# Optimization experiments

Hardware: AMD Instinct MI355X
Metric: run time of the kernel (lower is better)

## Reference

```python
import jax, jax.numpy as jnp
import numpy as np
import math

VOCAB = 128000
D_MODEL = 1024
CUTOFFS = [20000, 60000, VOCAB]  # cluster boundaries (last = vocab_size)
B, S = 8, 4096


def setup_inputs() -> dict:
    key = jax.random.key(0)
    ks = jax.random.split(key, 6)
    input_ids = jax.random.randint(ks[0], (B, S), 0, VOCAB)
    # cluster 0: ids [0, 20000), dim 1024, padding_idx=0 -> zero row
    emb0 = jax.random.normal(ks[1], (20000, 1024), jnp.float32)
    emb0 = emb0.at[0].set(0.0)
    # cluster 1: ids [20000, 60000), dim 256 (= 1024 // 4**1)
    emb1 = jax.random.normal(ks[2], (40000, 256), jnp.float32)
    # cluster 2: ids [60000, 128000), dim 64 (= 1024 // 4**2)
    emb2 = jax.random.normal(ks[3], (68000, 64), jnp.float32)
    # nn.Linear(emb_dim, d_model, bias=False): weight shape [d_model, emb_dim]
    proj1 = jax.random.normal(ks[4], (1024, 256), jnp.float32) * 0.02
    proj2 = jax.random.normal(ks[5], (1024, 64), jnp.float32) * 0.02
    return {"input_ids": input_ids, "emb0": emb0, "emb1": emb1, "emb2": emb2,
            "proj1": proj1, "proj2": proj2}


def reference(input_ids, emb0, emb1, emb2, proj1, proj2):
    d_model = emb0.shape[1]
    starts = [0, CUTOFFS[0], CUTOFFS[1]]
    ends = CUTOFFS
    tables = [emb0, emb1, emb2]
    projs = [None, proj1, proj2]
    out = jnp.zeros(input_ids.shape + (d_model,), jnp.float32)
    for start, end, tab, proj in zip(starts, ends, tables, projs):
        mask = (input_ids >= start) & (input_ids < end)          # [B,S]
        local = jnp.clip(input_ids - start, 0, tab.shape[0] - 1)  # in-range gather ids
        e = tab[local]                                            # [B,S,emb_dim]
        if proj is not None:
            e = jnp.einsum('bse,de->bsd', e, proj)                # project to d_model
        else:
            # padding_idx=0: row is zero; mask keeps grad out of row 0 too
            e = e * (input_ids != 0)[..., None].astype(e.dtype)
        out = out + jnp.where(mask[..., None], e, 0.0)            # masked scatter
    return out * math.sqrt(d_model)
```

## Files before the change

### kernel.cpp

```cpp
#include <hip/hip_runtime.h>
#include <hip/hip_bf16.h>


typedef __attribute__((ext_vector_type(4))) float        float4v;
typedef __attribute__((ext_vector_type(8))) short        short8;
typedef __attribute__((ext_vector_type(2))) unsigned int uint2v;

#define D_MODEL 1024

__device__ __forceinline__ short f2bf(float x) {
    unsigned u = __builtin_bit_cast(unsigned, x);
    unsigned r = u + 0x7fffu + ((u >> 16) & 1u);
    return (short)(r >> 16);
}

__device__ __forceinline__ uint2v pack4(float4v v) {
    uint2v r;
    r[0] = (unsigned)(unsigned short)f2bf(v[0]) | ((unsigned)(unsigned short)f2bf(v[1]) << 16);
    r[1] = (unsigned)(unsigned short)f2bf(v[2]) | ((unsigned)(unsigned short)f2bf(v[3]) << 16);
    return r;
}

__global__ __launch_bounds__(1024)
void prep_k(const int* __restrict__ ids, int n, int pb,
            int* __restrict__ cnt,
            int* __restrict__ l0, int* __restrict__ l1, int* __restrict__ l2,
            const float* __restrict__ proj1, const float* __restrict__ proj2,
            uint2v* __restrict__ p1bf, uint2v* __restrict__ p2bf)
{
    const int b = blockIdx.x;
    if (b >= pb) {
        int bb = b - pb;
        if (bb < 64) {
            int t = bb * 1024 + threadIdx.x;
            p1bf[t] = pack4(((const float4v*)proj1)[t]);
        } else {
            int t = (bb - 64) * 1024 + threadIdx.x;
            p2bf[t] = pack4(((const float4v*)proj2)[t]);
        }
        return;
    }

    __shared__ int s_wcnt[16][3];
    __shared__ int s_wbase[16][3];
    __shared__ int s_base[3];

    const int tid  = threadIdx.x;
    const int wave = tid >> 6;
    const int lane = tid & 63;
    const int i    = b * 1024 + tid;

    int id = (i < n) ? ids[i] : -1;
    bool is0 = (i < n) && (id < 20000);
    bool is1 = (i < n) && (id >= 20000) && (id < 60000);
    bool is2 = (i < n) && (id >= 60000);
    unsigned long long ltmask = (lane == 0) ? 0ull : (~0ull >> (64 - lane));

    unsigned long long m0 = __ballot(is0);
    unsigned long long m1 = __ballot(is1);
    unsigned long long m2 = __ballot(is2);
    if (lane == 0) {
        s_wcnt[wave][0] = __popcll(m0);
        s_wcnt[wave][1] = __popcll(m1);
        s_wcnt[wave][2] = __popcll(m2);
    }
    __syncthreads();

    if (tid < 3) {
        const int c = tid;
        int run = 0;
#pragma unroll
        for (int w = 0; w < 16; w++) { s_wbase[w][c] = run; run += s_wcnt[w][c]; }
        const int gidx = (c == 0) ? 2 : (c - 1);
        s_base[c] = atomicAdd(&cnt[gidx], run);
    }
    __syncthreads();

    if (is0) l0[s_base[0] + s_wbase[wave][0] + __popcll(m0 & ltmask)] = i;
    if (is1) l1[s_base[1] + s_wbase[wave][1] + __popcll(m1 & ltmask)] = i;
    if (is2) l2[s_base[2] + s_wbase[wave][2] + __popcll(m2 & ltmask)] = i;
}

template<int K, int START>
__device__ __forceinline__
void gemm_tile(int tile,
               const int* __restrict__ ids,
               const float* __restrict__ table,
               const short* __restrict__ pbf,
               const int* __restrict__ list,
               int count,
               float* __restrict__ out,
               int* s_tok, int* s_loc, short* s_a)
{
    constexpr int PK = K + 8;
    const int m_base = tile * 32;
    const int tid = threadIdx.x;
    if (tid < 32) {
        int m   = m_base + tid;
        int tok = (m < count) ? list[m] : -1;
        s_tok[tid] = tok;
        s_loc[tid] = (tok >= 0) ? (ids[tok] - START) : 0;
    }
    __syncthreads();

    {
        const int row = tid >> 4;
        const int c   = tid & 15;
        const float* src = table + (size_t)s_loc[row] * K + c * (K / 16);
        short*       dst = s_a + row * PK + c * (K / 16);
        if constexpr (K == 256) {
            const float4v* s4 = (const float4v*)src;
            float4v f0 = s4[0], f1 = s4[1], f2 = s4[2], f3 = s4[3];
            uint2v* d2 = (uint2v*)dst;
            d2[0] = pack4(f0); d2[1] = pack4(f1);
            d2[2] = pack4(f2); d2[3] = pack4(f3);
        } else {
            float4v f0 = *(const float4v*)src;
            *(uint2v*)dst = pack4(f0);
        }
    }
    __syncthreads();

    const int lane = tid & 63;
    const int wave = tid >> 6;
    const int col  = lane & 15;
    const int quad = lane >> 4;

    const short* arow0 = s_a + col * PK        + quad * 8;
    const short* arow1 = s_a + (col + 16) * PK + quad * 8;
    const short* bbase = pbf + (size_t)(wave * 128 + col) * K + quad * 8;

    float4v acc0[8], acc1[8];
#pragma unroll
    for (int i = 0; i < 8; i++) {
        acc0[i] = (float4v){0.f, 0.f, 0.f, 0.f};
        acc1[i] = (float4v){0.f, 0.f, 0.f, 0.f};
    }

#pragma unroll
    for (int ks = 0; ks < K; ks += 32) {
        short8 a0 = *(const short8*)(arow0 + ks);
        short8 a1 = *(const short8*)(arow1 + ks);
#pragma unroll
        for (int nt = 0; nt < 8; nt++) {
            short8 b = *(const short8*)(bbase + (size_t)nt * 16 * K + ks);
            acc0[nt] = __builtin_amdgcn_mfma_f32_16x16x32_bf16(a0, b, acc0[nt], 0, 0, 0);
            acc1[nt] = __builtin_amdgcn_mfma_f32_16x16x32_bf16(a1, b, acc1[nt], 0, 0, 0);
        }
    }

#pragma unroll
    for (int r = 0; r < 4; r++) {
        int row = quad * 4 + r;
        if (m_base + row < count) {
            float* orow = out + (size_t)s_tok[row] * D_MODEL + wave * 128 + col;
#pragma unroll
            for (int nt = 0; nt < 8; nt++) orow[nt * 16] = acc0[nt][r] * 32.0f;
        }
        if (m_base + 16 + row < count) {
            float* orow = out + (size_t)s_tok[16 + row] * D_MODEL + wave * 128 + col;
#pragma unroll
            for (int nt = 0; nt < 8; nt++) orow[nt * 16] = acc1[nt][r] * 32.0f;
        }
    }
    __syncthreads();
}

__device__ __forceinline__
void copy_item(int item, const int* __restrict__ ids,
               const int* __restrict__ l0, int count0,
               const float* __restrict__ emb0, float* __restrict__ out)
{
    int r = item * 2 + (threadIdx.x >> 8);
    if (r < count0) {
        int t  = l0[r];
        int id = ids[t];
        const float4v* src = (const float4v*)(emb0 + (size_t)id * D_MODEL);
        float4v*       dst = (float4v*)(out + (size_t)t * D_MODEL);
        int c = threadIdx.x & 255;
        dst[c] = src[c] * 32.0f;
    }
}

__global__ __launch_bounds__(512)
void fused_main(const int* __restrict__ ids,
                const float* __restrict__ emb0,
                const float* __restrict__ emb1,
                const float* __restrict__ emb2,
                const short* __restrict__ p1bf,
                const short* __restrict__ p2bf,
                const int* __restrict__ l0,
                const int* __restrict__ l1,
                const int* __restrict__ l2,
                const int* __restrict__ cnt,
                float* __restrict__ out)
{
    __shared__ int   s_tok[32];
    __shared__ int   s_loc[32];
    __shared__ short s_a[32 * 264];

    const int c1 = cnt[0];
    const int c2 = cnt[1];
    const int c0 = cnt[2];
    const int t1 = (c1 + 31) >> 5;
    const int t2 = (c2 + 31) >> 5;
    const int tc = (c0 + 1) >> 1;
    const int total = t1 + t2 + tc;

    for (int w = blockIdx.x; w < total; w += gridDim.x) {
        if (w < t1) {
            gemm_tile<256, 20000>(w, ids, emb1, p1bf, l1, c1, out, s_tok, s_loc, s_a);
        } else if (w < t1 + t2) {
            gemm_tile<64, 60000>(w - t1, ids, emb2, p2bf, l2, c2, out, s_tok, s_loc, s_a);
        } else {
            copy_item(w - t1 - t2, ids, l0, c0, emb0, out);
        }
    }
}

extern "C" void kernel_launch(void* const* d_in, const int* in_sizes, int n_in,
                              void* d_out, int out_size, void* d_ws, size_t ws_size,
                              hipStream_t stream)
{
    const int*   ids   = (const int*)  d_in[0];
    const float* emb0  = (const float*)d_in[1];
    const float* emb1  = (const float*)d_in[2];
    const float* emb2  = (const float*)d_in[3];
    const float* proj1 = (const float*)d_in[4];
    const float* proj2 = (const float*)d_in[5];
    float*       out   = (float*)d_out;
    const int n = in_sizes[0];

    int*   cnt  = (int*)d_ws;
    int*   l0   = (int*)((char*)d_ws + 256);
    int*   l1   = l0 + n;
    int*   l2   = l1 + n;
    size_t poff = (256 + (size_t)3 * n * 4 + 255) & ~(size_t)255;
    short* p1bf = (short*)((char*)d_ws + poff);
    short* p2bf = p1bf + 1024 * 256;

    const int pb = (n + 1023) / 1024;

    hipMemsetAsync(cnt, 0, 4 * sizeof(int), stream);
    prep_k<<<pb + 64 + 16, 1024, 0, stream>>>(ids, n, pb, cnt, l0, l1, l2,
                                              proj1, proj2,
                                              (uint2v*)p1bf, (uint2v*)p2bf);
    fused_main<<<2048, 512, 0, stream>>>(ids, emb0, emb1, emb2,
                                         p1bf, p2bf, l0, l1, l2, cnt, out);
}
```

Before: 272.8 us.

## Store (token, local id) pairs and split GEMM tiles into smaller 256-thread work items

The prep kernel now writes (token index, local row) pairs into the cluster lists, so the main kernel no longer re-reads input_ids for an indirect lookup. The main kernel moves to 256-thread blocks with launch_bounds(256,5). Each GEMM item now covers 16 tokens and half of the output columns, and each copy item has one wave handle one row with four float4 loads per lane. The aim is finer work granularity and higher occupancy, at the cost of loading each A tile twice (once per column half) and doubling list storage.

```diff
diff --git a/kernel.cpp b/kernel.cpp
--- a/kernel.cpp
+++ b/kernel.cpp
@@ -5,6 +5,7 @@
 typedef __attribute__((ext_vector_type(4))) float        float4v;
 typedef __attribute__((ext_vector_type(8))) short        short8;
 typedef __attribute__((ext_vector_type(2))) unsigned int uint2v;
+typedef __attribute__((ext_vector_type(2))) int          int2v;
 
 #define D_MODEL 1024
 
@@ -24,7 +25,7 @@
 __global__ __launch_bounds__(1024)
 void prep_k(const int* __restrict__ ids, int n, int pb,
             int* __restrict__ cnt,
-            int* __restrict__ l0, int* __restrict__ l1, int* __restrict__ l2,
+            int2v* __restrict__ l0, int2v* __restrict__ l1, int2v* __restrict__ l2,
             const float* __restrict__ proj1, const float* __restrict__ proj2,
             uint2v* __restrict__ p1bf, uint2v* __restrict__ p2bf)
 {
@@ -76,37 +77,34 @@
     }
     __syncthreads();
 
-    if (is0) l0[s_base[0] + s_wbase[wave][0] + __popcll(m0 & ltmask)] = i;
-    if (is1) l1[s_base[1] + s_wbase[wave][1] + __popcll(m1 & ltmask)] = i;
-    if (is2) l2[s_base[2] + s_wbase[wave][2] + __popcll(m2 & ltmask)] = i;
-}
-
-template<int K, int START>
+    if (is0) l0[s_base[0] + s_wbase[wave][0] + __popcll(m0 & ltmask)] = (int2v){i, id};
+    if (is1) l1[s_base[1] + s_wbase[wave][1] + __popcll(m1 & ltmask)] = (int2v){i, id - 20000};
+    if (is2) l2[s_base[2] + s_wbase[wave][2] + __popcll(m2 & ltmask)] = (int2v){i, id - 60000};
+}
+
+template<int K>
 __device__ __forceinline__
-void gemm_tile(int tile,
-               const int* __restrict__ ids,
+void gemm_item(int tile, int dimh,
                const float* __restrict__ table,
                const short* __restrict__ pbf,
-               const int* __restrict__ list,
+               const int2v* __restrict__ list,
                int count,
                float* __restrict__ out,
-               int* s_tok, int* s_loc, short* s_a)
+               int2v* s_tl, short* s_a)
 {
     constexpr int PK = K + 8;
-    const int m_base = tile * 32;
+    const int m_base = tile * 16;
     const int tid = threadIdx.x;
-    if (tid < 32) {
-        int m   = m_base + tid;
-        int tok = (m < count) ? list[m] : -1;
-        s_tok[tid] = tok;
-        s_loc[tid] = (tok >= 0) ? (ids[tok] - START) : 0;
+    if (tid < 16) {
+        int m = m_base + tid;
+        s_tl[tid] = (m < count) ? list[m] : (int2v){-1, 0};
     }
     __syncthreads();
 
     {
         const int row = tid >> 4;
         const int c   = tid & 15;
-        const float* src = table + (size_t)s_loc[row] * K + c * (K / 16);
+        const float* src = table + (size_t)s_tl[row][1] * K + c * (K / 16);
         short*       dst = s_a + row * PK + c * (K / 16);
         if constexpr (K == 256) {
             const float4v* s4 = (const float4v*)src;
@@ -125,27 +123,22 @@
     const int wave = tid >> 6;
     const int col  = lane & 15;
     const int quad = lane >> 4;
-
-    const short* arow0 = s_a + col * PK        + quad * 8;
-    const short* arow1 = s_a + (col + 16) * PK + quad * 8;
-    const short* bbase = pbf + (size_t)(wave * 128 + col) * K + quad * 8;
-
-    float4v acc0[8], acc1[8];
-#pragma unroll
-    for (int i = 0; i < 8; i++) {
-        acc0[i] = (float4v){0.f, 0.f, 0.f, 0.f};
-        acc1[i] = (float4v){0.f, 0.f, 0.f, 0.f};
-    }
+    const int nb   = dimh * 512 + wave * 128;
+
+    const short* arow  = s_a + col * PK + quad * 8;
+    const short* bbase = pbf + (size_t)(nb + col) * K + quad * 8;
+
+    float4v acc[8];
+#pragma unroll
+    for (int i = 0; i < 8; i++) acc[i] = (float4v){0.f, 0.f, 0.f, 0.f};
 
 #pragma unroll
     for (int ks = 0; ks < K; ks += 32) {
-        short8 a0 = *(const short8*)(arow0 + ks);
-        short8 a1 = *(const short8*)(arow1 + ks);
+        short8 a = *(const short8*)(arow + ks);
 #pragma unroll
         for (int nt = 0; nt < 8; nt++) {
             short8 b = *(const short8*)(bbase + (size_t)nt * 16 * K + ks);
-            acc0[nt] = __builtin_amdgcn_mfma_f32_16x16x32_bf16(a0, b, acc0[nt], 0, 0, 0);
-            acc1[nt] = __builtin_amdgcn_mfma_f32_16x16x32_bf16(a1, b, acc1[nt], 0, 0, 0);
+            acc[nt] = __builtin_amdgcn_mfma_f32_16x16x32_bf16(a, b, acc[nt], 0, 0, 0);
         }
     }
 
@@ -153,67 +146,63 @@
     for (int r = 0; r < 4; r++) {
         int row = quad * 4 + r;
         if (m_base + row < count) {
-            float* orow = out + (size_t)s_tok[row] * D_MODEL + wave * 128 + col;
-#pragma unroll
-            for (int nt = 0; nt < 8; nt++) orow[nt * 16] = acc0[nt][r] * 32.0f;
-        }
-        if (m_base + 16 + row < count) {
-            float* orow = out + (size_t)s_tok[16 + row] * D_MODEL + wave * 128 + col;
-#pragma unroll
-            for (int nt = 0; nt < 8; nt++) orow[nt * 16] = acc1[nt][r] * 32.0f;
+            float* orow = out + (size_t)s_tl[row][0] * D_MODEL + nb + col;
+#pragma unroll
+            for (int nt = 0; nt < 8; nt++) orow[nt * 16] = acc[nt][r] * 32.0f;
         }
     }
     __syncthreads();
 }
 
 __device__ __forceinline__
-void copy_item(int item, const int* __restrict__ ids,
-               const int* __restrict__ l0, int count0,
+void copy_item(int item, const int2v* __restrict__ l0, int count0,
                const float* __restrict__ emb0, float* __restrict__ out)
 {
-    int r = item * 2 + (threadIdx.x >> 8);
+    int r = item * 4 + (threadIdx.x >> 6);
     if (r < count0) {
-        int t  = l0[r];
-        int id = ids[t];
-        const float4v* src = (const float4v*)(emb0 + (size_t)id * D_MODEL);
-        float4v*       dst = (float4v*)(out + (size_t)t * D_MODEL);
-        int c = threadIdx.x & 255;
-        dst[c] = src[c] * 32.0f;
-    }
-}
-
-__global__ __launch_bounds__(512)
-void fused_main(const int* __restrict__ ids,
-                const float* __restrict__ emb0,
+        int2v tl = l0[r];
+        const float4v* src = (const float4v*)(emb0 + (size_t)tl[1] * D_MODEL);
+        float4v*       dst = (float4v*)(out + (size_t)tl[0] * D_MODEL);
+        int c = threadIdx.x & 63;
+        float4v v0 = src[c], v1 = src[c + 64], v2 = src[c + 128], v3 = src[c + 192];
+        dst[c]       = v0 * 32.0f;
+        dst[c + 64]  = v1 * 32.0f;
+        dst[c + 128] = v2 * 32.0f;
+        dst[c + 192] = v3 * 32.0f;
+    }
+}
+
+__global__ __launch_bounds__(256, 5)
+void fused_main(const float* __restrict__ emb0,
                 const float* __restrict__ emb1,
                 const float* __restrict__ emb2,
                 const short* __restrict__ p1bf,
                 const short* __restrict__ p2bf,
-                const int* __restrict__ l0,
-                const int* __restrict__ l1,
-                const int* __restrict__ l2,
+                const int2v* __restrict__ l0,
+                const int2v* __restrict__ l1,
+                const int2v* __restrict__ l2,
                 const int* __restrict__ cnt,
                 float* __restrict__ out)
 {
-    __shared__ int   s_tok[32];
-    __shared__ int   s_loc[32];
-    __shared__ short s_a[32 * 264];
+    __shared__ int2v s_tl[16];
+    __shared__ short s_a[16 * 264];
 
     const int c1 = cnt[0];
     const int c2 = cnt[1];
     const int c0 = cnt[2];
-    const int t1 = (c1 + 31) >> 5;
-    const int t2 = (c2 + 31) >> 5;
-    const int tc = (c0 + 1) >> 1;
-    const int total = t1 + t2 + tc;
+    const int g1 = ((c1 + 15) >> 4) * 2;
+    const int g2 = ((c2 + 15) >> 4) * 2;
+    const int tc = (c0 + 3) >> 2;
+    const int total = g1 + g2 + tc;
 
     for (int w = blockIdx.x; w < total; w += gridDim.x) {
-        if (w < t1) {
-            gemm_tile<256, 20000>(w, ids, emb1, p1bf, l1, c1, out, s_tok, s_loc, s_a);
-        } else if (w < t1 + t2) {
-            gemm_tile<64, 60000>(w - t1, ids, emb2, p2bf, l2, c2, out, s_tok, s_loc, s_a);
+        if (w < g1) {
+            gemm_item<256>(w >> 1, w & 1, emb1, p1bf, l1, c1, out, s_tl, s_a);
+        } else if (w < g1 + g2) {
+            int u = w - g1;
+            gemm_item<64>(u >> 1, u & 1, emb2, p2bf, l2, c2, out, s_tl, s_a);
         } else {
-            copy_item(w - t1 - t2, ids, l0, c0, emb0, out);
+            copy_item(w - g1 - g2, l0, c0, emb0, out);
         }
     }
 }
@@ -232,10 +221,10 @@
     const int n = in_sizes[0];
 
     int*   cnt  = (int*)d_ws;
-    int*   l0   = (int*)((char*)d_ws + 256);
-    int*   l1   = l0 + n;
-    int*   l2   = l1 + n;
-    size_t poff = (256 + (size_t)3 * n * 4 + 255) & ~(size_t)255;
+    int2v* l0   = (int2v*)((char*)d_ws + 256);
+    int2v* l1   = l0 + n;
+    int2v* l2   = l1 + n;
+    size_t poff = (256 + (size_t)3 * n * 8 + 255) & ~(size_t)255;
     short* p1bf = (short*)((char*)d_ws + poff);
     short* p2bf = p1bf + 1024 * 256;
 
@@ -245,6 +234,6 @@
     prep_k<<<pb + 64 + 16, 1024, 0, stream>>>(ids, n, pb, cnt, l0, l1, l2,
                                               proj1, proj2,
                                               (uint2v*)p1bf, (uint2v*)p2bf);
-    fused_main<<<2048, 512, 0, stream>>>(ids, emb0, emb1, emb2,
+    fused_main<<<4096, 256, 0, stream>>>(emb0, emb1, emb2,
                                          p1bf, p2bf, l0, l1, l2, cnt, out);
 }
```

Result: slower. 289.4 us (+6.1%).
